# Kernel optimization log

Hardware: AMD Instinct MI355X
Metric: run time of the kernel (lower is better)

Reference implementation:

```python
import jax, jax.numpy as jnp
import numpy as np

B, L, H, ED, NCONV = 64, 2048, 128, 4, 3
N = B * L


def gat(x, src, dst, edge_attr, W, a_s, a_d, We, a_e, b, self_loops):
    """PyG GATConv, heads=1, concat=True, negative_slope=0.2, fill_value='mean'."""
    n = x.shape[0]
    h = x @ W                              # [N,H]
    a_src = h @ a_s                        # [N]
    a_dst = h @ a_d                        # [N]
    alpha = a_src[src] + a_dst[dst] + (edge_attr @ We) @ a_e  # [E]
    if self_loops:
        ones = jnp.ones(src.shape[0], x.dtype)
        deg = jax.ops.segment_sum(ones, dst, num_segments=n)
        mean_attr = jax.ops.segment_sum(edge_attr, dst, num_segments=n) / jnp.maximum(deg, 1.0)[:, None]
        loop_alpha = a_src + a_dst + (mean_attr @ We) @ a_e
        idx = jnp.arange(n, dtype=src.dtype)
        src = jnp.concatenate([src, idx])
        dst = jnp.concatenate([dst, idx])
        alpha = jnp.concatenate([alpha, loop_alpha])
    alpha = jax.nn.leaky_relu(alpha, 0.2)
    m = jax.ops.segment_max(alpha, dst, num_segments=n)
    ex = jnp.exp(alpha - m[dst])
    den = jax.ops.segment_sum(ex, dst, num_segments=n)
    coef = ex / jnp.maximum(den, 1e-16)[dst]
    return jax.ops.segment_sum(coef[:, None] * h[src], dst, num_segments=n) + b


def setup_inputs() -> dict:
    key = jax.random.key(0)
    ks = iter(jax.random.split(key, 32))
    # binary trees: per graph, node k>0 has parent (k-1)//2; edge child->parent (to_up)
    local = np.arange(1, L)
    parent = (local - 1) // 2
    offs = (np.arange(B) * L)[:, None]
    src = jnp.asarray((local[None, :] + offs).ravel(), dtype=jnp.int32)
    dst = jnp.asarray((parent[None, :] + offs).ravel(), dtype=jnp.int32)
    E = src.shape[0]
    s = 0.1
    inp = {
        "x": jax.random.normal(next(ks), (N,), jnp.float32),
        "src": src,
        "dst": dst,
        "edge_attr": jax.random.normal(next(ks), (E, ED), jnp.float32),
        "up_W0": jax.random.normal(next(ks), (1, H)) * s,
        "up_W": jax.random.normal(next(ks), (NCONV - 1, H, H)) * s,
        "up_att_src": jax.random.normal(next(ks), (NCONV, H)) * s,
        "up_att_dst": jax.random.normal(next(ks), (NCONV, H)) * s,
        "up_We": jax.random.normal(next(ks), (NCONV, ED, H)) * s,
        "up_att_edge": jax.random.normal(next(ks), (NCONV, H)) * s,
        "up_b": jax.random.normal(next(ks), (NCONV, H)) * s,
        "down_W": jax.random.normal(next(ks), (NCONV - 1, H, H)) * s,
        "down_att_src": jax.random.normal(next(ks), (NCONV - 1, H)) * s,
        "down_att_dst": jax.random.normal(next(ks), (NCONV - 1, H)) * s,
        "down_We": jax.random.normal(next(ks), (NCONV - 1, ED, H)) * s,
        "down_att_edge": jax.random.normal(next(ks), (NCONV - 1, H)) * s,
        "down_b": jax.random.normal(next(ks), (NCONV - 1, H)) * s,
        "lin_W": jax.random.normal(next(ks), (NCONV - 1, H, H)) * s,
        "lin_b": jax.random.normal(next(ks), (NCONV - 1, H)) * s,
        "lin_last_W": jax.random.normal(next(ks), (H, 1)) * s,
        "lin_last_b": jax.random.normal(next(ks), (1,)) * s,
    }
    return inp


def reference(x, src, dst, edge_attr, up_W0, up_W, up_att_src, up_att_dst, up_We,
              up_att_edge, up_b, down_W, down_att_src, down_att_dst, down_We,
              down_att_edge, down_b, lin_W, lin_b, lin_last_W, lin_last_b):
    h = x[:, None]                                            # flat_c.view(-1,1)
    # upward pass: toup GATConvs (with self loops) + relu
    for i in range(NCONV):
        W = up_W0 if i == 0 else up_W[i - 1]
        h = jax.nn.relu(gat(h, src, dst, edge_attr, W, up_att_src[i], up_att_dst[i],
                            up_We[i], up_att_edge[i], up_b[i], True))
    x_up = h
    # downward pass uses reversed edges, no self loops; replicates original's
    # indexing bug (todown[0] used twice, todown[-1] never used)
    src_d, dst_d = dst, src
    x_down = jax.nn.relu(gat(x_up, src_d, dst_d, edge_attr, down_W[0], down_att_src[0],
                             down_att_dst[0], down_We[0], down_att_edge[0], down_b[0], False))
    xx = x_down + x_up
    for i in range(NCONV - 1):
        xx = jax.nn.relu(xx @ lin_W[i] + lin_b[i])
        x_down = jax.nn.relu(gat(xx, src_d, dst_d, edge_attr, down_W[i], down_att_src[i],
                                 down_att_dst[i], down_We[i], down_att_edge[i], down_b[i], False))
        xx = x_down + x_up
    final_emb = xx
    out_nodes = xx @ lin_last_W + lin_last_b                  # [N,1]
    batch_out = out_nodes.reshape(B, L)                       # all graphs are max_len
    batch_emb = final_emb.reshape(B, L, H)
    out = batch_out - batch_out[:, :1]                        # subtract root node
    return out, batch_emb
```

## Files before the change

kernel.cpp:

```cpp
#include <hip/hip_runtime.h>
#include <hip/hip_bf16.h>
#include <cstdint>
#include <cstddef>

typedef unsigned short u16;
typedef short bf16x8 __attribute__((ext_vector_type(8)));
typedef float f32x4 __attribute__((ext_vector_type(4)));

#define Bn 64
#define Ln 2048
#define Hn 128
#define EDn 4
#define Nn (Bn*Ln)

#define CV_W0    0
#define CV_WUP   128
#define CV_AS    32896
#define CV_AD    33280
#define CV_WE    33664
#define CV_AE    35200
#define CV_BUP   35584
#define CV_WD    35968
#define CV_BD    68736
#define CV_WL    68992
#define CV_BL    101760
#define CV_WLAST 102016
#define CV_TOTAL 102144

__device__ __forceinline__ float b2f(u16 u) {
  union { float f; unsigned int i; } v; v.i = ((unsigned int)u) << 16; return v.f;
}
__device__ __forceinline__ u16 f2b(float f) {
  __hip_bfloat16 h = __float2bfloat16(f);
  union { __hip_bfloat16 h; u16 u; } v; v.h = h; return v.u;
}
__device__ __forceinline__ float lrelu(float v) { return v >= 0.f ? v : 0.2f * v; }
__device__ __forceinline__ float wave_sum(float r) {
  #pragma unroll
  for (int off = 32; off > 0; off >>= 1) r += __shfl_xor(r, off, 64);
  return r;
}
__device__ __forceinline__ float ld_in(const void* p, size_t i, int f) {
  return f ? b2f(((const u16*)p)[i]) : ((const float*)p)[i];
}
__device__ __forceinline__ u16* Cbase(void* dout, int f) {
  return f ? ((u16*)dout + Nn) : (u16*)((float*)dout + Nn);
}
__device__ __forceinline__ float lo16(unsigned v) { return b2f((u16)(v & 0xFFFF)); }
__device__ __forceinline__ float hi16(unsigned v) { return b2f((u16)(v >> 16)); }

__global__ void detect_kernel(const u16* __restrict__ x, int* __restrict__ flag) {
  int lane = threadIdx.x;
  u16 u = x[lane];
  int e = (u >> 7) & 0xFF;
  bool good = (e >= 100 && e <= 140) || ((u & 0x7FFF) == 0);
  unsigned long long m = __ballot(good);
  if (lane == 0) *flag = (__popcll(m) >= 56) ? 1 : 0;
}

struct CvtArgs { const void* src[12]; int off[12]; int tr[12]; };
__global__ void cvt_kernel(CvtArgs a, const int* __restrict__ flagp, u16* __restrict__ dst) {
  int f = *flagp;
  int i = blockIdx.x * 256 + threadIdx.x;
  if (i >= CV_TOTAL) return;
  int s = 0;
  #pragma unroll
  for (int k = 1; k < 12; ++k) s = (i >= a.off[k]) ? k : s;
  int j = i - a.off[s];
  int sj = j;
  if (a.tr[s]) {
    int mat = j >> 14, rr = (j >> 7) & 127, cc = j & 127;
    sj = (mat << 14) + cc * 128 + rr;
  }
  dst[i] = f ? ((const u16*)a.src[s])[sj] : f2b(((const float*)a.src[s])[sj]);
}

__global__ void up0_kernel(const void* __restrict__ x, const void* __restrict__ edge_attr,
                           const u16* __restrict__ W0, const u16* __restrict__ att_s,
                           const u16* __restrict__ att_d, const u16* __restrict__ We0,
                           const u16* __restrict__ ae0, const u16* __restrict__ b0,
                           u16* __restrict__ y, const int* __restrict__ flagp) {
  __shared__ float P[6];
  __shared__ float comb[64];
  __shared__ float W0s[Hn];
  __shared__ float b0s[Hn];
  int f = *flagp;
  int t = threadIdx.x;
  int lane = t & 63, w = t >> 6;
  if (w < 2) {
    const u16* vb = (w == 0) ? att_s : att_d;
    float r = b2f(W0[lane]) * b2f(vb[lane]) + b2f(W0[lane+64]) * b2f(vb[lane+64]);
    r = wave_sum(r);
    if (lane == 0) P[w] = r;
  } else {
    int e0 = (w - 2) * 2;
    float a0 = b2f(ae0[lane]), a1 = b2f(ae0[lane+64]);
    float r0 = b2f(We0[e0*Hn+lane])*a0     + b2f(We0[e0*Hn+lane+64])*a1;
    float r1 = b2f(We0[(e0+1)*Hn+lane])*a0 + b2f(We0[(e0+1)*Hn+lane+64])*a1;
    r0 = wave_sum(r0); r1 = wave_sum(r1);
    if (lane == 0) { P[2+e0] = r0; P[3+e0] = r1; }
  }
  if (t < Hn) { W0s[t] = b2f(W0[t]); b0s[t] = b2f(b0[t]); }
  __syncthreads();
  int base = blockIdx.x * 64;
  if (t < 64) {
    int n = base + t;
    int local = n & (Ln - 1);
    int nb = n >> 11;
    int root = n - local;
    float S0 = P[0], D0 = P[1];
    float w0 = P[2], w1 = P[3], w2 = P[4], w3 = P[5];
    float xp = ld_in(x, n, f);
    float ad_p = D0 * xp;
    int c1l = 2*local + 1, c2l = 2*local + 2;
    int deg = (c1l < Ln ? 1 : 0) + (c2l < Ln ? 1 : 0);
    float e1 = 0.f, e2 = 0.f, xc1 = 0.f, xc2 = 0.f, sc1 = 0.f, sc2 = 0.f;
    if (deg >= 1) {
      xc1 = ld_in(x, root + c1l, f);
      size_t ei = ((size_t)nb*(Ln-1) + (c1l-1))*EDn;
      e1 = ld_in(edge_attr, ei+0, f)*w0 + ld_in(edge_attr, ei+1, f)*w1
         + ld_in(edge_attr, ei+2, f)*w2 + ld_in(edge_attr, ei+3, f)*w3;
      sc1 = lrelu(S0*xc1 + ad_p + e1);
    }
    if (deg == 2) {
      xc2 = ld_in(x, root + c2l, f);
      size_t ei = ((size_t)nb*(Ln-1) + (c2l-1))*EDn;
      e2 = ld_in(edge_attr, ei+0, f)*w0 + ld_in(edge_attr, ei+1, f)*w1
         + ld_in(edge_attr, ei+2, f)*w2 + ld_in(edge_attr, ei+3, f)*w3;
      sc2 = lrelu(S0*xc2 + ad_p + e2);
    }
    float mean_e = deg ? (e1 + e2) / (float)deg : 0.f;
    float ss = lrelu(S0*xp + ad_p + mean_e);
    float m = ss;
    if (deg >= 1) m = fmaxf(m, sc1);
    if (deg == 2) m = fmaxf(m, sc2);
    float es  = __expf(ss - m);
    float ec1 = (deg >= 1) ? __expf(sc1 - m) : 0.f;
    float ec2 = (deg == 2) ? __expf(sc2 - m) : 0.f;
    float den = es + ec1 + ec2;
    comb[t] = (es*xp + ec1*xc1 + ec2*xc2) / den;
  }
  __syncthreads();
  u16* out = y + (size_t)base * Hn;
  for (int i = t; i < 64*Hn/4; i += 256) {
    int row = i >> 5;
    int col = (i & 31) * 4;
    float c = comb[row];
    ushort4 st;
    st.x = f2b(fmaxf(c*W0s[col+0] + b0s[col+0], 0.f));
    st.y = f2b(fmaxf(c*W0s[col+1] + b0s[col+1], 0.f));
    st.z = f2b(fmaxf(c*W0s[col+2] + b0s[col+2], 0.f));
    st.w = f2b(fmaxf(c*W0s[col+3] + b0s[col+3], 0.f));
    *(ushort4*)&out[(size_t)i*4] = st;
  }
}

template<int GATHER, int EPI, int ASAD>
__global__ __launch_bounds__(256, 2) void gemm_k(
                       const u16* __restrict__ Xp, const u16* __restrict__ Wt,
                       const u16* __restrict__ bias, const u16* __restrict__ Uarr,
                       u16* __restrict__ outp, void* __restrict__ dout,
                       const int* __restrict__ flagp, int x_is_C, int out_mode,
                       float2* __restrict__ asad, const u16* __restrict__ avs,
                       const u16* __restrict__ avd, float* __restrict__ nodesp) {
  __shared__ u16 Ws[Hn*Hn];
  int f = *flagp;
  const u16* X = x_is_C ? Cbase(dout, f) : Xp;
  int t = threadIdx.x;
  int lane = t & 63, w = t >> 6;
  int m = lane & 15, q = lane >> 4;
  int row0 = blockIdx.x * 256;
  int wbase = row0 + w*64;
  uint4 xf[4][4];
  #pragma unroll
  for (int rt = 0; rt < 4; ++rt) {
    int R = wbase + rt*16 + m;
    bool zero = false;
    const uint4* src;
    if (GATHER) {
      int local = R & (Ln - 1);
      if (local == 0) { zero = true; src = (const uint4*)X; }
      else src = (const uint4*)(X + (size_t)((R - local) + ((local - 1) >> 1))*Hn);
    } else {
      src = (const uint4*)(X + (size_t)R*Hn);
    }
    #pragma unroll
    for (int ki = 0; ki < 4; ++ki) {
      uint4 v = src[ki*4 + q];
      if (zero) { v.x = 0; v.y = 0; v.z = 0; v.w = 0; }
      xf[rt][ki] = v;
    }
  }
  #pragma unroll
  for (int i = 0; i < 8; ++i) {
    int g = t + 256*i; int r = g >> 4, u = g & 15;
    uint4 v = ((const uint4*)Wt)[g];
    *(uint4*)&Ws[(r*16 + (u ^ (r & 15)))*8] = v;
  }
  __syncthreads();
  f32x4 acc[4][8];
  #pragma unroll
  for (int rt = 0; rt < 4; ++rt)
    #pragma unroll
    for (int ct = 0; ct < 8; ++ct) acc[rt][ct] = (f32x4){0.f, 0.f, 0.f, 0.f};
  #pragma unroll
  for (int ki = 0; ki < 4; ++ki) {
    #pragma unroll
    for (int ct = 0; ct < 8; ++ct) {
      bf16x8 wf = *(bf16x8*)&Ws[((ct*16 + m)*16 + ((ki*4 + q) ^ m))*8];
      #pragma unroll
      for (int rt = 0; rt < 4; ++rt)
        acc[rt][ct] = __builtin_amdgcn_mfma_f32_16x16x32_bf16(
                        wf, *(bf16x8*)&xf[rt][ki], acc[rt][ct], 0, 0, 0);
    }
  }
  u16* Cb = Cbase(dout, f);
  float* emf = (float*)dout + Nn;
  u16* od = (out_mode == 0) ? outp : (out_mode == 1 ? Cb : (u16*)dout + Nn);
  #pragma unroll
  for (int rt = 0; rt < 4; ++rt) {
    int R = wbase + rt*16 + m;
    float asv = 0.f, adv = 0.f;
    #pragma unroll
    for (int ct = 0; ct < 8; ++ct) {
      int c0 = ct*16 + q*4;
      float o[4];
      #pragma unroll
      for (int r = 0; r < 4; ++r) o[r] = acc[rt][ct][r];
      if (ASAD == 1) {
        ushort4 sv = *(const ushort4*)&avs[c0];
        ushort4 dv = *(const ushort4*)&avd[c0];
        asv += o[0]*b2f(sv.x) + o[1]*b2f(sv.y) + o[2]*b2f(sv.z) + o[3]*b2f(sv.w);
        adv += o[0]*b2f(dv.x) + o[1]*b2f(dv.y) + o[2]*b2f(dv.z) + o[3]*b2f(dv.w);
      }
      if (EPI >= 1) {
        ushort4 bv = *(const ushort4*)&bias[c0];
        o[0] = fmaxf(o[0] + b2f(bv.x), 0.f); o[1] = fmaxf(o[1] + b2f(bv.y), 0.f);
        o[2] = fmaxf(o[2] + b2f(bv.z), 0.f); o[3] = fmaxf(o[3] + b2f(bv.w), 0.f);
      }
      if (EPI == 2) {
        ushort4 uv = *(const ushort4*)&Uarr[(size_t)R*Hn + c0];
        o[0] += b2f(uv.x); o[1] += b2f(uv.y); o[2] += b2f(uv.z); o[3] += b2f(uv.w);
      }
      if (ASAD == 2) {
        ushort4 sv = *(const ushort4*)&avs[c0];
        asv += o[0]*b2f(sv.x) + o[1]*b2f(sv.y) + o[2]*b2f(sv.z) + o[3]*b2f(sv.w);
      }
      if (out_mode == 2 && !f) {
        float4 fv; fv.x = o[0]; fv.y = o[1]; fv.z = o[2]; fv.w = o[3];
        *(float4*)&emf[(size_t)R*Hn + c0] = fv;
      } else {
        ushort4 st; st.x = f2b(o[0]); st.y = f2b(o[1]); st.z = f2b(o[2]); st.w = f2b(o[3]);
        *(ushort4*)&od[(size_t)R*Hn + c0] = st;
      }
    }
    if (ASAD == 1) {
      asv += __shfl_xor(asv, 16, 64); asv += __shfl_xor(asv, 32, 64);
      adv += __shfl_xor(adv, 16, 64); adv += __shfl_xor(adv, 32, 64);
      if (q == 0) { float2 v; v.x = asv; v.y = adv; asad[R] = v; }
    }
    if (ASAD == 2) {
      asv += __shfl_xor(asv, 16, 64); asv += __shfl_xor(asv, 32, 64);
      if (q == 0) nodesp[R] = asv;
    }
  }
}

__global__ __launch_bounds__(256, 2) void gemm_blend_k(
                       const u16* __restrict__ Wt, const float2* __restrict__ coef,
                       const u16* __restrict__ bias_up, u16* __restrict__ outp,
                       void* __restrict__ dout, const int* __restrict__ flagp,
                       float2* __restrict__ asad, const u16* __restrict__ avs,
                       const u16* __restrict__ avd) {
  __shared__ u16 Ws[Hn*Hn];
  int f = *flagp;
  const u16* h = Cbase(dout, f);
  int t = threadIdx.x;
  int lane = t & 63, w = t >> 6;
  int m = lane & 15, q = lane >> 4;
  int row0 = blockIdx.x * 256;
  int wbase = row0 + w*64;
  uint4 xf[4][4];
  #pragma unroll
  for (int rt = 0; rt < 4; ++rt) {
    int R = wbase + rt*16 + m;
    int local = R & (Ln - 1);
    int root = R - local;
    int c1l = 2*local + 1, c2l = 2*local + 2;
    int r1 = (c1l < Ln) ? root + c1l : R;
    int r2 = (c2l < Ln) ? root + c2l : R;
    float2 cf = coef[R];
    float es = 1.f - cf.x - cf.y;
    const uint4* hp = (const uint4*)(h + (size_t)R*Hn);
    const uint4* h1 = (const uint4*)(h + (size_t)r1*Hn);
    const uint4* h2 = (const uint4*)(h + (size_t)r2*Hn);
    #pragma unroll
    for (int ki = 0; ki < 4; ++ki) {
      int u = ki*4 + q;
      uint4 a = hp[u], b = h1[u], c = h2[u];
      uint4 bv = ((const uint4*)bias_up)[u];
      uint4 st;
      #pragma unroll
      for (int i = 0; i < 4; ++i) {
        unsigned av = ((unsigned*)&a)[i], b1v = ((unsigned*)&b)[i];
        unsigned b2v = ((unsigned*)&c)[i], bbv = ((unsigned*)&bv)[i];
        float o0 = es*lo16(av) + cf.x*lo16(b1v) + cf.y*lo16(b2v) + lo16(bbv);
        float o1 = es*hi16(av) + cf.x*hi16(b1v) + cf.y*hi16(b2v) + hi16(bbv);
        ((unsigned*)&st)[i] = (unsigned)f2b(fmaxf(o0, 0.f))
                            | ((unsigned)f2b(fmaxf(o1, 0.f)) << 16);
      }
      xf[rt][ki] = st;
    }
  }
  #pragma unroll
  for (int i = 0; i < 8; ++i) {
    int g = t + 256*i; int r = g >> 4, u = g & 15;
    uint4 v = ((const uint4*)Wt)[g];
    *(uint4*)&Ws[(r*16 + (u ^ (r & 15)))*8] = v;
  }
  __syncthreads();
  f32x4 acc[4][8];
  #pragma unroll
  for (int rt = 0; rt < 4; ++rt)
    #pragma unroll
    for (int ct = 0; ct < 8; ++ct) acc[rt][ct] = (f32x4){0.f, 0.f, 0.f, 0.f};
  #pragma unroll
  for (int ki = 0; ki < 4; ++ki) {
    #pragma unroll
    for (int ct = 0; ct < 8; ++ct) {
      bf16x8 wf = *(bf16x8*)&Ws[((ct*16 + m)*16 + ((ki*4 + q) ^ m))*8];
      #pragma unroll
      for (int rt = 0; rt < 4; ++rt)
        acc[rt][ct] = __builtin_amdgcn_mfma_f32_16x16x32_bf16(
                        wf, *(bf16x8*)&xf[rt][ki], acc[rt][ct], 0, 0, 0);
    }
  }
  #pragma unroll
  for (int rt = 0; rt < 4; ++rt) {
    int R = wbase + rt*16 + m;
    float asv = 0.f, adv = 0.f;
    #pragma unroll
    for (int ct = 0; ct < 8; ++ct) {
      int c0 = ct*16 + q*4;
      float o0 = acc[rt][ct][0], o1 = acc[rt][ct][1];
      float o2 = acc[rt][ct][2], o3 = acc[rt][ct][3];
      ushort4 sv = *(const ushort4*)&avs[c0];
      ushort4 dv = *(const ushort4*)&avd[c0];
      asv += o0*b2f(sv.x) + o1*b2f(sv.y) + o2*b2f(sv.z) + o3*b2f(sv.w);
      adv += o0*b2f(dv.x) + o1*b2f(dv.y) + o2*b2f(dv.z) + o3*b2f(dv.w);
      ushort4 st; st.x = f2b(o0); st.y = f2b(o1); st.z = f2b(o2); st.w = f2b(o3);
      *(ushort4*)&outp[(size_t)R*Hn + c0] = st;
    }
    asv += __shfl_xor(asv, 16, 64); asv += __shfl_xor(asv, 32, 64);
    adv += __shfl_xor(adv, 16, 64); adv += __shfl_xor(adv, 32, 64);
    if (q == 0) { float2 v; v.x = asv; v.y = adv; asad[R] = v; }
  }
}

__global__ __launch_bounds__(256, 2) void fused_down_lin_k(
                       const u16* __restrict__ Xp, const u16* __restrict__ Wdt,
                       const u16* __restrict__ bd, const u16* __restrict__ Uarr,
                       const u16* __restrict__ Wlt, const u16* __restrict__ bl,
                       u16* __restrict__ outp) {
  __shared__ u16 Ws[Hn*Hn];
  __shared__ u16 XX[128*Hn];
  int t = threadIdx.x;
  int lane = t & 63, w = t >> 6;
  int m = lane & 15, q = lane >> 4;
  int row0 = blockIdx.x * 128;
  int wbase = row0 + w*32;
  uint4 xf[2][4];
  #pragma unroll
  for (int rt = 0; rt < 2; ++rt) {
    int R = wbase + rt*16 + m;
    int local = R & (Ln - 1);
    bool zero = (local == 0);
    const uint4* src = zero ? (const uint4*)Xp
                     : (const uint4*)(Xp + (size_t)((R - local) + ((local - 1) >> 1))*Hn);
    #pragma unroll
    for (int ki = 0; ki < 4; ++ki) {
      uint4 v = src[ki*4 + q];
      if (zero) { v.x = 0; v.y = 0; v.z = 0; v.w = 0; }
      xf[rt][ki] = v;
    }
  }
  #pragma unroll
  for (int i = 0; i < 8; ++i) {
    int g = t + 256*i; int r = g >> 4, u = g & 15;
    uint4 v = ((const uint4*)Wdt)[g];
    *(uint4*)&Ws[(r*16 + (u ^ (r & 15)))*8] = v;
  }
  __syncthreads();
  f32x4 acc[2][8];
  #pragma unroll
  for (int rt = 0; rt < 2; ++rt)
    #pragma unroll
    for (int ct = 0; ct < 8; ++ct) acc[rt][ct] = (f32x4){0.f, 0.f, 0.f, 0.f};
  #pragma unroll
  for (int ki = 0; ki < 4; ++ki) {
    #pragma unroll
    for (int ct = 0; ct < 8; ++ct) {
      bf16x8 wf = *(bf16x8*)&Ws[((ct*16 + m)*16 + ((ki*4 + q) ^ m))*8];
      #pragma unroll
      for (int rt = 0; rt < 2; ++rt)
        acc[rt][ct] = __builtin_amdgcn_mfma_f32_16x16x32_bf16(
                        wf, *(bf16x8*)&xf[rt][ki], acc[rt][ct], 0, 0, 0);
    }
  }
  __syncthreads();
  #pragma unroll
  for (int rt = 0; rt < 2; ++rt) {
    int R = wbase + rt*16 + m;
    int rl = w*32 + rt*16 + m;
    #pragma unroll
    for (int ct = 0; ct < 8; ++ct) {
      int c0 = ct*16 + q*4;
      ushort4 bv = *(const ushort4*)&bd[c0];
      ushort4 uv = *(const ushort4*)&Uarr[(size_t)R*Hn + c0];
      float o0 = fmaxf(acc[rt][ct][0] + b2f(bv.x), 0.f) + b2f(uv.x);
      float o1 = fmaxf(acc[rt][ct][1] + b2f(bv.y), 0.f) + b2f(uv.y);
      float o2 = fmaxf(acc[rt][ct][2] + b2f(bv.z), 0.f) + b2f(uv.z);
      float o3 = fmaxf(acc[rt][ct][3] + b2f(bv.w), 0.f) + b2f(uv.w);
      int uu = (2*ct + (q >> 1)) ^ m;
      uint2 pk;
      pk.x = (unsigned)f2b(o0) | ((unsigned)f2b(o1) << 16);
      pk.y = (unsigned)f2b(o2) | ((unsigned)f2b(o3) << 16);
      *(uint2*)&XX[rl*Hn + uu*8 + (q & 1)*4] = pk;
    }
  }
  #pragma unroll
  for (int i = 0; i < 8; ++i) {
    int g = t + 256*i; int r = g >> 4, u = g & 15;
    uint4 v = ((const uint4*)Wlt)[g];
    *(uint4*)&Ws[(r*16 + (u ^ (r & 15)))*8] = v;
  }
  __syncthreads();
  f32x4 acc2[2][8];
  #pragma unroll
  for (int rt = 0; rt < 2; ++rt)
    #pragma unroll
    for (int ct = 0; ct < 8; ++ct) acc2[rt][ct] = (f32x4){0.f, 0.f, 0.f, 0.f};
  #pragma unroll
  for (int ki = 0; ki < 4; ++ki) {
    #pragma unroll
    for (int ct = 0; ct < 8; ++ct) {
      bf16x8 wf = *(bf16x8*)&Ws[((ct*16 + m)*16 + ((ki*4 + q) ^ m))*8];
      #pragma unroll
      for (int rt = 0; rt < 2; ++rt) {
        int rl = w*32 + rt*16 + m;
        bf16x8 xb = *(bf16x8*)&XX[rl*Hn + (((ki*4 + q) ^ m))*8];
        acc2[rt][ct] = __builtin_amdgcn_mfma_f32_16x16x32_bf16(wf, xb, acc2[rt][ct], 0, 0, 0);
      }
    }
  }
  #pragma unroll
  for (int rt = 0; rt < 2; ++rt) {
    int R = wbase + rt*16 + m;
    #pragma unroll
    for (int ct = 0; ct < 8; ++ct) {
      int c0 = ct*16 + q*4;
      ushort4 bv = *(const ushort4*)&bl[c0];
      ushort4 st;
      st.x = f2b(fmaxf(acc2[rt][ct][0] + b2f(bv.x), 0.f));
      st.y = f2b(fmaxf(acc2[rt][ct][1] + b2f(bv.y), 0.f));
      st.z = f2b(fmaxf(acc2[rt][ct][2] + b2f(bv.z), 0.f));
      st.w = f2b(fmaxf(acc2[rt][ct][3] + b2f(bv.w), 0.f));
      *(ushort4*)&outp[(size_t)R*Hn + c0] = st;
    }
  }
}

__global__ void coef_kernel(const void* __restrict__ edge_attr,
                            const u16* __restrict__ We, const u16* __restrict__ ae,
                            const float2* __restrict__ asad, float2* __restrict__ coef,
                            const int* __restrict__ flagp) {
  __shared__ float P[4];
  int f = *flagp;
  int t = threadIdx.x;
  int lane = t & 63, w = t >> 6;
  {
    unsigned av = *(const unsigned*)&ae[2*lane];
    unsigned wv = *(const unsigned*)&We[w*Hn + 2*lane];
    float r = wave_sum(lo16(wv)*lo16(av) + hi16(wv)*hi16(av));
    if (lane == 0) P[w] = r;
  }
  __syncthreads();
  int p = blockIdx.x * 256 + t;
  int local = p & (Ln - 1);
  int root = p - local;
  int nb = p >> 11;
  int c1l = 2*local + 1, c2l = 2*local + 2;
  int deg = (c1l < Ln ? 1 : 0) + (c2l < Ln ? 1 : 0);
  float2 aa = asad[p];
  float w0 = P[0], w1 = P[1], w2 = P[2], w3 = P[3];
  float e1 = 0.f, e2 = 0.f, sc1 = 0.f, sc2 = 0.f;
  if (deg >= 1) {
    size_t ei = ((size_t)nb*(Ln-1) + (c1l-1))*EDn;
    if (f) {
      ushort4 v = *(const ushort4*)((const u16*)edge_attr + ei);
      e1 = b2f(v.x)*w0 + b2f(v.y)*w1 + b2f(v.z)*w2 + b2f(v.w)*w3;
      if (deg == 2) {
        ushort4 v2 = *(const ushort4*)((const u16*)edge_attr + ei + EDn);
        e2 = b2f(v2.x)*w0 + b2f(v2.y)*w1 + b2f(v2.z)*w2 + b2f(v2.w)*w3;
      }
    } else {
      float4 v = *(const float4*)((const float*)edge_attr + ei);
      e1 = v.x*w0 + v.y*w1 + v.z*w2 + v.w*w3;
      if (deg == 2) {
        float4 v2 = *(const float4*)((const float*)edge_attr + ei + EDn);
        e2 = v2.x*w0 + v2.y*w1 + v2.z*w2 + v2.w*w3;
      }
    }
    sc1 = lrelu(asad[root + c1l].x + aa.y + e1);
    if (deg == 2) sc2 = lrelu(asad[root + c2l].x + aa.y + e2);
  }
  float mean_e = deg ? (e1 + e2) / (float)deg : 0.f;
  float ss = lrelu(aa.x + aa.y + mean_e);
  float m = ss;
  if (deg >= 1) m = fmaxf(m, sc1);
  if (deg == 2) m = fmaxf(m, sc2);
  float es  = __expf(ss - m);
  float ec1 = (deg >= 1) ? __expf(sc1 - m) : 0.f;
  float ec2 = (deg == 2) ? __expf(sc2 - m) : 0.f;
  float inv = 1.f / (es + ec1 + ec2);
  float2 cf; cf.x = ec1 * inv; cf.y = ec2 * inv;
  coef[p] = cf;
}

__global__ void blend_kernel(const u16* __restrict__ h, const float2* __restrict__ coef,
                             const u16* __restrict__ bias, u16* __restrict__ y) {
  int t = threadIdx.x;
  int g = t & 15;
  int p = blockIdx.x * 16 + (t >> 4);
  int local = p & (Ln - 1);
  int root = p - local;
  int c1l = 2*local + 1, c2l = 2*local + 2;
  int deg = (c1l < Ln ? 1 : 0) + (c2l < Ln ? 1 : 0);
  float2 cf = coef[p];
  float es = 1.f - cf.x - cf.y;
  int off = g * 8;
  uint4 hp = *(const uint4*)&h[(size_t)p*Hn + off];
  uint4 h1 = {0,0,0,0}, h2 = {0,0,0,0};
  if (deg >= 1) h1 = *(const uint4*)&h[(size_t)(root + c1l)*Hn + off];
  if (deg == 2) h2 = *(const uint4*)&h[(size_t)(root + c2l)*Hn + off];
  uint4 bv = *(const uint4*)&bias[off];
  uint4 st;
  #pragma unroll
  for (int i = 0; i < 4; ++i) {
    unsigned a = ((unsigned*)&hp)[i], b1 = ((unsigned*)&h1)[i];
    unsigned b2 = ((unsigned*)&h2)[i], bb = ((unsigned*)&bv)[i];
    float o0 = es*lo16(a) + cf.x*lo16(b1) + cf.y*lo16(b2) + lo16(bb);
    float o1 = es*hi16(a) + cf.x*hi16(b1) + cf.y*hi16(b2) + hi16(bb);
    ((unsigned*)&st)[i] = (unsigned)f2b(fmaxf(o0, 0.f)) | ((unsigned)f2b(fmaxf(o1, 0.f)) << 16);
  }
  *(uint4*)&y[(size_t)p*Hn + off] = st;
}

__global__ void score_kernel(const float* __restrict__ nodes, void* __restrict__ dout,
                             const int* __restrict__ flagp) {
  int f = *flagp;
  int n = blockIdx.x * 256 + threadIdx.x;
  float v = nodes[n] - nodes[n & ~(Ln - 1)];
  if (f) ((u16*)dout)[n] = f2b(v);
  else   ((float*)dout)[n] = v;
}

extern "C" void kernel_launch(void* const* d_in, const int* in_sizes, int n_in,
                              void* d_out, int out_size, void* d_ws, size_t ws_size,
                              hipStream_t stream) {
  const void* x         = d_in[0];
  const void* edge_attr = d_in[3];

  u16* Ubuf = (u16*)d_ws;
  u16* Abuf = Ubuf + (size_t)Nn*Hn;
  u16* Bbuf = Abuf + (size_t)Nn*Hn;
  u16* cvt  = Bbuf + (size_t)Nn*Hn;
  float2* asad = (float2*)(cvt + CV_TOTAL);
  float2* coef = asad + Nn;
  float* nodes = (float*)(coef + Nn);
  int* flag = (int*)(nodes + Nn);

  detect_kernel<<<1, 64, 0, stream>>>((const u16*)d_in[0], flag);

  CvtArgs ca;
  ca.src[0]  = d_in[4];  ca.off[0]  = CV_W0;    ca.tr[0]  = 0;
  ca.src[1]  = d_in[5];  ca.off[1]  = CV_WUP;   ca.tr[1]  = 1;
  ca.src[2]  = d_in[6];  ca.off[2]  = CV_AS;    ca.tr[2]  = 0;
  ca.src[3]  = d_in[7];  ca.off[3]  = CV_AD;    ca.tr[3]  = 0;
  ca.src[4]  = d_in[8];  ca.off[4]  = CV_WE;    ca.tr[4]  = 0;
  ca.src[5]  = d_in[9];  ca.off[5]  = CV_AE;    ca.tr[5]  = 0;
  ca.src[6]  = d_in[10]; ca.off[6]  = CV_BUP;   ca.tr[6]  = 0;
  ca.src[7]  = d_in[11]; ca.off[7]  = CV_WD;    ca.tr[7]  = 1;
  ca.src[8]  = d_in[16]; ca.off[8]  = CV_BD;    ca.tr[8]  = 0;
  ca.src[9]  = d_in[17]; ca.off[9]  = CV_WL;    ca.tr[9]  = 1;
  ca.src[10] = d_in[18]; ca.off[10] = CV_BL;    ca.tr[10] = 0;
  ca.src[11] = d_in[19]; ca.off[11] = CV_WLAST; ca.tr[11] = 0;
  cvt_kernel<<<(CV_TOTAL + 255)/256, 256, 0, stream>>>(ca, flag, cvt);

  up0_kernel<<<Nn/64, 256, 0, stream>>>(x, edge_attr, cvt+CV_W0, cvt+CV_AS, cvt+CV_AD,
                                        cvt+CV_WE, cvt+CV_AE, cvt+CV_BUP, Abuf, flag);
  gemm_k<0,0,1><<<Nn/256, 256, 0, stream>>>(Abuf, cvt+CV_WUP, nullptr, nullptr,
                                         nullptr, d_out, flag, 0, 1,
                                         asad, cvt+CV_AS+Hn, cvt+CV_AD+Hn, nullptr);
  coef_kernel<<<Nn/256, 256, 0, stream>>>(edge_attr, cvt+CV_WE+EDn*Hn, cvt+CV_AE+Hn,
                                          asad, coef, flag);
  gemm_blend_k<<<Nn/256, 256, 0, stream>>>(cvt+CV_WUP+Hn*Hn, coef, cvt+CV_BUP+Hn,
                                           Bbuf, d_out, flag,
                                           asad, cvt+CV_AS+2*Hn, cvt+CV_AD+2*Hn);
  coef_kernel<<<Nn/256, 256, 0, stream>>>(edge_attr, cvt+CV_WE+2*EDn*Hn, cvt+CV_AE+2*Hn,
                                          asad, coef, flag);
  blend_kernel<<<Nn/16, 256, 0, stream>>>(Bbuf, coef, cvt+CV_BUP+2*Hn, Ubuf);

  fused_down_lin_k<<<Nn/128, 256, 0, stream>>>(Ubuf, cvt+CV_WD, cvt+CV_BD, Ubuf,
                                               cvt+CV_WL, cvt+CV_BL, Abuf);
  fused_down_lin_k<<<Nn/128, 256, 0, stream>>>(Abuf, cvt+CV_WD, cvt+CV_BD, Ubuf,
                                               cvt+CV_WL+Hn*Hn, cvt+CV_BL+Hn, Bbuf);
  gemm_k<1,2,2><<<Nn/256, 256, 0, stream>>>(Bbuf, cvt+CV_WD+Hn*Hn, cvt+CV_BD+Hn, Ubuf,
                                         nullptr, d_out, flag, 0, 2,
                                         nullptr, cvt+CV_WLAST, nullptr, nodes);

  score_kernel<<<Nn/256, 256, 0, stream>>>(nodes, d_out, flag);
}
```

Before: 266.0 us.

## Shrink GEMM row tiles, split column accumulation, prefetch weights into registers

The node GEMM kernels now process 128 rows per block instead of 256, with two 16-row tiles per wave. Columns are accumulated in two halves so fewer accumulator registers are live, and launch bounds rise to allow four blocks per CU. Weight tiles are loaded into registers before the activation gather, so their latency overlaps the gather instead of following it. The fused down/lin kernel moves to 512 threads with one 16-row tile per wave and prefetches the second weight matrix during the first epilogue. The cost is that each block now loads the shared 32KB weight tile for half as many rows, and register pressure under the tighter bounds could cause spills.

```diff
diff --git a/kernel.cpp b/kernel.cpp
--- a/kernel.cpp
+++ b/kernel.cpp
@@ -156,7 +156,7 @@
 }
 
 template<int GATHER, int EPI, int ASAD>
-__global__ __launch_bounds__(256, 2) void gemm_k(
+__global__ __launch_bounds__(256, 4) void gemm_k(
                        const u16* __restrict__ Xp, const u16* __restrict__ Wt,
                        const u16* __restrict__ bias, const u16* __restrict__ Uarr,
                        u16* __restrict__ outp, void* __restrict__ dout,
@@ -169,11 +169,14 @@
   int t = threadIdx.x;
   int lane = t & 63, w = t >> 6;
   int m = lane & 15, q = lane >> 4;
-  int row0 = blockIdx.x * 256;
-  int wbase = row0 + w*64;
-  uint4 xf[4][4];
-  #pragma unroll
-  for (int rt = 0; rt < 4; ++rt) {
+  int row0 = blockIdx.x * 128;
+  int wbase = row0 + w*32;
+  uint4 wstage[8];
+  #pragma unroll
+  for (int i = 0; i < 8; ++i) wstage[i] = ((const uint4*)Wt)[t + 256*i];
+  uint4 xf[2][4];
+  #pragma unroll
+  for (int rt = 0; rt < 2; ++rt) {
     int R = wbase + rt*16 + m;
     bool zero = false;
     const uint4* src;
@@ -194,79 +197,89 @@
   #pragma unroll
   for (int i = 0; i < 8; ++i) {
     int g = t + 256*i; int r = g >> 4, u = g & 15;
-    uint4 v = ((const uint4*)Wt)[g];
-    *(uint4*)&Ws[(r*16 + (u ^ (r & 15)))*8] = v;
-  }
-  __syncthreads();
-  f32x4 acc[4][8];
-  #pragma unroll
-  for (int rt = 0; rt < 4; ++rt)
-    #pragma unroll
-    for (int ct = 0; ct < 8; ++ct) acc[rt][ct] = (f32x4){0.f, 0.f, 0.f, 0.f};
-  #pragma unroll
-  for (int ki = 0; ki < 4; ++ki) {
-    #pragma unroll
-    for (int ct = 0; ct < 8; ++ct) {
-      bf16x8 wf = *(bf16x8*)&Ws[((ct*16 + m)*16 + ((ki*4 + q) ^ m))*8];
-      #pragma unroll
-      for (int rt = 0; rt < 4; ++rt)
-        acc[rt][ct] = __builtin_amdgcn_mfma_f32_16x16x32_bf16(
-                        wf, *(bf16x8*)&xf[rt][ki], acc[rt][ct], 0, 0, 0);
-    }
-  }
+    *(uint4*)&Ws[(r*16 + (u ^ (r & 15)))*8] = wstage[i];
+  }
+  __syncthreads();
   u16* Cb = Cbase(dout, f);
   float* emf = (float*)dout + Nn;
   u16* od = (out_mode == 0) ? outp : (out_mode == 1 ? Cb : (u16*)dout + Nn);
-  #pragma unroll
-  for (int rt = 0; rt < 4; ++rt) {
+  float asv[2] = {0.f, 0.f}, adv[2] = {0.f, 0.f};
+  #pragma unroll
+  for (int cb = 0; cb < 2; ++cb) {
+    f32x4 acc[2][4];
+    #pragma unroll
+    for (int rt = 0; rt < 2; ++rt)
+      #pragma unroll
+      for (int c4 = 0; c4 < 4; ++c4) acc[rt][c4] = (f32x4){0.f, 0.f, 0.f, 0.f};
+    #pragma unroll
+    for (int ki = 0; ki < 4; ++ki) {
+      #pragma unroll
+      for (int c4 = 0; c4 < 4; ++c4) {
+        int ct = cb*4 + c4;
+        bf16x8 wf = *(bf16x8*)&Ws[((ct*16 + m)*16 + ((ki*4 + q) ^ m))*8];
+        #pragma unroll
+        for (int rt = 0; rt < 2; ++rt)
+          acc[rt][c4] = __builtin_amdgcn_mfma_f32_16x16x32_bf16(
+                          wf, *(bf16x8*)&xf[rt][ki], acc[rt][c4], 0, 0, 0);
+      }
+    }
+    #pragma unroll
+    for (int rt = 0; rt < 2; ++rt) {
+      int R = wbase + rt*16 + m;
+      #pragma unroll
+      for (int c4 = 0; c4 < 4; ++c4) {
+        int ct = cb*4 + c4;
+        int c0 = ct*16 + q*4;
+        float o[4];
+        #pragma unroll
+        for (int r = 0; r < 4; ++r) o[r] = acc[rt][c4][r];
+        if (ASAD == 1) {
+          ushort4 sv = *(const ushort4*)&avs[c0];
+          ushort4 dv = *(const ushort4*)&avd[c0];
+          asv[rt] += o[0]*b2f(sv.x) + o[1]*b2f(sv.y) + o[2]*b2f(sv.z) + o[3]*b2f(sv.w);
+          adv[rt] += o[0]*b2f(dv.x) + o[1]*b2f(dv.y) + o[2]*b2f(dv.z) + o[3]*b2f(dv.w);
+        }
+        if (EPI >= 1) {
+          ushort4 bv = *(const ushort4*)&bias[c0];
+          o[0] = fmaxf(o[0] + b2f(bv.x), 0.f); o[1] = fmaxf(o[1] + b2f(bv.y), 0.f);
+          o[2] = fmaxf(o[2] + b2f(bv.z), 0.f); o[3] = fmaxf(o[3] + b2f(bv.w), 0.f);
+        }
+        if (EPI == 2) {
+          ushort4 uv = *(const ushort4*)&Uarr[(size_t)R*Hn + c0];
+          o[0] += b2f(uv.x); o[1] += b2f(uv.y); o[2] += b2f(uv.z); o[3] += b2f(uv.w);
+        }
+        if (ASAD == 2) {
+          ushort4 sv = *(const ushort4*)&avs[c0];
+          asv[rt] += o[0]*b2f(sv.x) + o[1]*b2f(sv.y) + o[2]*b2f(sv.z) + o[3]*b2f(sv.w);
+        }
+        if (out_mode == 2 && !f) {
+          float4 fv; fv.x = o[0]; fv.y = o[1]; fv.z = o[2]; fv.w = o[3];
+          *(float4*)&emf[(size_t)R*Hn + c0] = fv;
+        } else {
+          ushort4 st; st.x = f2b(o[0]); st.y = f2b(o[1]); st.z = f2b(o[2]); st.w = f2b(o[3]);
+          *(ushort4*)&od[(size_t)R*Hn + c0] = st;
+        }
+      }
+    }
+  }
+  #pragma unroll
+  for (int rt = 0; rt < 2; ++rt) {
     int R = wbase + rt*16 + m;
-    float asv = 0.f, adv = 0.f;
-    #pragma unroll
-    for (int ct = 0; ct < 8; ++ct) {
-      int c0 = ct*16 + q*4;
-      float o[4];
-      #pragma unroll
-      for (int r = 0; r < 4; ++r) o[r] = acc[rt][ct][r];
-      if (ASAD == 1) {
-        ushort4 sv = *(const ushort4*)&avs[c0];
-        ushort4 dv = *(const ushort4*)&avd[c0];
-        asv += o[0]*b2f(sv.x) + o[1]*b2f(sv.y) + o[2]*b2f(sv.z) + o[3]*b2f(sv.w);
-        adv += o[0]*b2f(dv.x) + o[1]*b2f(dv.y) + o[2]*b2f(dv.z) + o[3]*b2f(dv.w);
-      }
-      if (EPI >= 1) {
-        ushort4 bv = *(const ushort4*)&bias[c0];
-        o[0] = fmaxf(o[0] + b2f(bv.x), 0.f); o[1] = fmaxf(o[1] + b2f(bv.y), 0.f);
-        o[2] = fmaxf(o[2] + b2f(bv.z), 0.f); o[3] = fmaxf(o[3] + b2f(bv.w), 0.f);
-      }
-      if (EPI == 2) {
-        ushort4 uv = *(const ushort4*)&Uarr[(size_t)R*Hn + c0];
-        o[0] += b2f(uv.x); o[1] += b2f(uv.y); o[2] += b2f(uv.z); o[3] += b2f(uv.w);
-      }
-      if (ASAD == 2) {
-        ushort4 sv = *(const ushort4*)&avs[c0];
-        asv += o[0]*b2f(sv.x) + o[1]*b2f(sv.y) + o[2]*b2f(sv.z) + o[3]*b2f(sv.w);
-      }
-      if (out_mode == 2 && !f) {
-        float4 fv; fv.x = o[0]; fv.y = o[1]; fv.z = o[2]; fv.w = o[3];
-        *(float4*)&emf[(size_t)R*Hn + c0] = fv;
-      } else {
-        ushort4 st; st.x = f2b(o[0]); st.y = f2b(o[1]); st.z = f2b(o[2]); st.w = f2b(o[3]);
-        *(ushort4*)&od[(size_t)R*Hn + c0] = st;
-      }
-    }
     if (ASAD == 1) {
-      asv += __shfl_xor(asv, 16, 64); asv += __shfl_xor(asv, 32, 64);
-      adv += __shfl_xor(adv, 16, 64); adv += __shfl_xor(adv, 32, 64);
-      if (q == 0) { float2 v; v.x = asv; v.y = adv; asad[R] = v; }
+      float as_ = asv[rt], ad_ = adv[rt];
+      as_ += __shfl_xor(as_, 16, 64); as_ += __shfl_xor(as_, 32, 64);
+      ad_ += __shfl_xor(ad_, 16, 64); ad_ += __shfl_xor(ad_, 32, 64);
+      if (q == 0) { float2 v; v.x = as_; v.y = ad_; asad[R] = v; }
     }
     if (ASAD == 2) {
-      asv += __shfl_xor(asv, 16, 64); asv += __shfl_xor(asv, 32, 64);
-      if (q == 0) nodesp[R] = asv;
-    }
-  }
-}
-
-__global__ __launch_bounds__(256, 2) void gemm_blend_k(
+      float as_ = asv[rt];
+      as_ += __shfl_xor(as_, 16, 64); as_ += __shfl_xor(as_, 32, 64);
+      if (q == 0) nodesp[R] = as_;
+    }
+  }
+}
+
+__global__ __launch_bounds__(256, 4) void gemm_blend_k(
                        const u16* __restrict__ Wt, const float2* __restrict__ coef,
                        const u16* __restrict__ bias_up, u16* __restrict__ outp,
                        void* __restrict__ dout, const int* __restrict__ flagp,
@@ -278,11 +291,14 @@
   int t = threadIdx.x;
   int lane = t & 63, w = t >> 6;
   int m = lane & 15, q = lane >> 4;
-  int row0 = blockIdx.x * 256;
-  int wbase = row0 + w*64;
-  uint4 xf[4][4];
-  #pragma unroll
-  for (int rt = 0; rt < 4; ++rt) {
+  int row0 = blockIdx.x * 128;
+  int wbase = row0 + w*32;
+  uint4 wstage[8];
+  #pragma unroll
+  for (int i = 0; i < 8; ++i) wstage[i] = ((const uint4*)Wt)[t + 256*i];
+  uint4 xf[2][4];
+  #pragma unroll
+  for (int rt = 0; rt < 2; ++rt) {
     int R = wbase + rt*16 + m;
     int local = R & (Ln - 1);
     int root = R - local;
@@ -315,49 +331,58 @@
   #pragma unroll
   for (int i = 0; i < 8; ++i) {
     int g = t + 256*i; int r = g >> 4, u = g & 15;
-    uint4 v = ((const uint4*)Wt)[g];
-    *(uint4*)&Ws[(r*16 + (u ^ (r & 15)))*8] = v;
-  }
-  __syncthreads();
-  f32x4 acc[4][8];
-  #pragma unroll
-  for (int rt = 0; rt < 4; ++rt)
-    #pragma unroll
-    for (int ct = 0; ct < 8; ++ct) acc[rt][ct] = (f32x4){0.f, 0.f, 0.f, 0.f};
-  #pragma unroll
-  for (int ki = 0; ki < 4; ++ki) {
-    #pragma unroll
-    for (int ct = 0; ct < 8; ++ct) {
-      bf16x8 wf = *(bf16x8*)&Ws[((ct*16 + m)*16 + ((ki*4 + q) ^ m))*8];
+    *(uint4*)&Ws[(r*16 + (u ^ (r & 15)))*8] = wstage[i];
+  }
+  __syncthreads();
+  float asv[2] = {0.f, 0.f}, adv[2] = {0.f, 0.f};
+  #pragma unroll
+  for (int cb = 0; cb < 2; ++cb) {
+    f32x4 acc[2][4];
+    #pragma unroll
+    for (int rt = 0; rt < 2; ++rt)
       #pragma unroll
-      for (int rt = 0; rt < 4; ++rt)
-        acc[rt][ct] = __builtin_amdgcn_mfma_f32_16x16x32_bf16(
-                        wf, *(bf16x8*)&xf[rt][ki], acc[rt][ct], 0, 0, 0);
-    }
-  }
-  #pragma unroll
-  for (int rt = 0; rt < 4; ++rt) {
+      for (int c4 = 0; c4 < 4; ++c4) acc[rt][c4] = (f32x4){0.f, 0.f, 0.f, 0.f};
+    #pragma unroll
+    for (int ki = 0; ki < 4; ++ki) {
+      #pragma unroll
+      for (int c4 = 0; c4 < 4; ++c4) {
+        int ct = cb*4 + c4;
+        bf16x8 wf = *(bf16x8*)&Ws[((ct*16 + m)*16 + ((ki*4 + q) ^ m))*8];
+        #pragma unroll
+        for (int rt = 0; rt < 2; ++rt)
+          acc[rt][c4] = __builtin_amdgcn_mfma_f32_16x16x32_bf16(
+                          wf, *(bf16x8*)&xf[rt][ki], acc[rt][c4], 0, 0, 0);
+      }
+    }
+    #pragma unroll
+    for (int rt = 0; rt < 2; ++rt) {
+      int R = wbase + rt*16 + m;
+      #pragma unroll
+      for (int c4 = 0; c4 < 4; ++c4) {
+        int ct = cb*4 + c4;
+        int c0 = ct*16 + q*4;
+        float o0 = acc[rt][c4][0], o1 = acc[rt][c4][1];
+        float o2 = acc[rt][c4][2], o3 = acc[rt][c4][3];
+        ushort4 sv = *(const ushort4*)&avs[c0];
+        ushort4 dv = *(const ushort4*)&avd[c0];
+        asv[rt] += o0*b2f(sv.x) + o1*b2f(sv.y) + o2*b2f(sv.z) + o3*b2f(sv.w);
+        adv[rt] += o0*b2f(dv.x) + o1*b2f(dv.y) + o2*b2f(dv.z) + o3*b2f(dv.w);
+        ushort4 st; st.x = f2b(o0); st.y = f2b(o1); st.z = f2b(o2); st.w = f2b(o3);
+        *(ushort4*)&outp[(size_t)R*Hn + c0] = st;
+      }
+    }
+  }
+  #pragma unroll
+  for (int rt = 0; rt < 2; ++rt) {
     int R = wbase + rt*16 + m;
-    float asv = 0.f, adv = 0.f;
-    #pragma unroll
-    for (int ct = 0; ct < 8; ++ct) {
-      int c0 = ct*16 + q*4;
-      float o0 = acc[rt][ct][0], o1 = acc[rt][ct][1];
-      float o2 = acc[rt][ct][2], o3 = acc[rt][ct][3];
-      ushort4 sv = *(const ushort4*)&avs[c0];
-      ushort4 dv = *(const ushort4*)&avd[c0];
-      asv += o0*b2f(sv.x) + o1*b2f(sv.y) + o2*b2f(sv.z) + o3*b2f(sv.w);
-      adv += o0*b2f(dv.x) + o1*b2f(dv.y) + o2*b2f(dv.z) + o3*b2f(dv.w);
-      ushort4 st; st.x = f2b(o0); st.y = f2b(o1); st.z = f2b(o2); st.w = f2b(o3);
-      *(ushort4*)&outp[(size_t)R*Hn + c0] = st;
-    }
-    asv += __shfl_xor(asv, 16, 64); asv += __shfl_xor(asv, 32, 64);
-    adv += __shfl_xor(adv, 16, 64); adv += __shfl_xor(adv, 32, 64);
-    if (q == 0) { float2 v; v.x = asv; v.y = adv; asad[R] = v; }
-  }
-}
-
-__global__ __launch_bounds__(256, 2) void fused_down_lin_k(
+    float as_ = asv[rt], ad_ = adv[rt];
+    as_ += __shfl_xor(as_, 16, 64); as_ += __shfl_xor(as_, 32, 64);
+    ad_ += __shfl_xor(ad_, 16, 64); ad_ += __shfl_xor(ad_, 32, 64);
+    if (q == 0) { float2 v; v.x = as_; v.y = ad_; asad[R] = v; }
+  }
+}
+
+__global__ __launch_bounds__(512, 4) void fused_down_lin_k(
                        const u16* __restrict__ Xp, const u16* __restrict__ Wdt,
                        const u16* __restrict__ bd, const u16* __restrict__ Uarr,
                        const u16* __restrict__ Wlt, const u16* __restrict__ bl,
@@ -368,11 +393,13 @@
   int lane = t & 63, w = t >> 6;
   int m = lane & 15, q = lane >> 4;
   int row0 = blockIdx.x * 128;
-  int wbase = row0 + w*32;
-  uint4 xf[2][4];
-  #pragma unroll
-  for (int rt = 0; rt < 2; ++rt) {
-    int R = wbase + rt*16 + m;
+  int R = row0 + w*16 + m;
+  int rl = w*16 + m;
+  uint4 wstage[4];
+  #pragma unroll
+  for (int i = 0; i < 4; ++i) wstage[i] = ((const uint4*)Wdt)[t + 512*i];
+  uint4 xf[4];
+  {
     int local = R & (Ln - 1);
     bool zero = (local == 0);
     const uint4* src = zero ? (const uint4*)Xp
@@ -381,92 +408,73 @@
     for (int ki = 0; ki < 4; ++ki) {
       uint4 v = src[ki*4 + q];
       if (zero) { v.x = 0; v.y = 0; v.z = 0; v.w = 0; }
-      xf[rt][ki] = v;
-    }
-  }
-  #pragma unroll
-  for (int i = 0; i < 8; ++i) {
-    int g = t + 256*i; int r = g >> 4, u = g & 15;
-    uint4 v = ((const uint4*)Wdt)[g];
-    *(uint4*)&Ws[(r*16 + (u ^ (r & 15)))*8] = v;
-  }
-  __syncthreads();
-  f32x4 acc[2][8];
-  #pragma unroll
-  for (int rt = 0; rt < 2; ++rt)
-    #pragma unroll
-    for (int ct = 0; ct < 8; ++ct) acc[rt][ct] = (f32x4){0.f, 0.f, 0.f, 0.f};
+      xf[ki] = v;
+    }
+  }
+  #pragma unroll
+  for (int i = 0; i < 4; ++i) {
+    int g = t + 512*i; int r = g >> 4, u = g & 15;
+    *(uint4*)&Ws[(r*16 + (u ^ (r & 15)))*8] = wstage[i];
+  }
+  __syncthreads();
+  f32x4 acc[8];
+  #pragma unroll
+  for (int ct = 0; ct < 8; ++ct) acc[ct] = (f32x4){0.f, 0.f, 0.f, 0.f};
   #pragma unroll
   for (int ki = 0; ki < 4; ++ki) {
     #pragma unroll
     for (int ct = 0; ct < 8; ++ct) {
       bf16x8 wf = *(bf16x8*)&Ws[((ct*16 + m)*16 + ((ki*4 + q) ^ m))*8];
-      #pragma unroll
-      for (int rt = 0; rt < 2; ++rt)
-        acc[rt][ct] = __builtin_amdgcn_mfma_f32_16x16x32_bf16(
-                        wf, *(bf16x8*)&xf[rt][ki], acc[rt][ct], 0, 0, 0);
-    }
-  }
-  __syncthreads();
-  #pragma unroll
-  for (int rt = 0; rt < 2; ++rt) {
-    int R = wbase + rt*16 + m;
-    int rl = w*32 + rt*16 + m;
-    #pragma unroll
-    for (int ct = 0; ct < 8; ++ct) {
-      int c0 = ct*16 + q*4;
-      ushort4 bv = *(const ushort4*)&bd[c0];
-      ushort4 uv = *(const ushort4*)&Uarr[(size_t)R*Hn + c0];
-      float o0 = fmaxf(acc[rt][ct][0] + b2f(bv.x), 0.f) + b2f(uv.x);
-      float o1 = fmaxf(acc[rt][ct][1] + b2f(bv.y), 0.f) + b2f(uv.y);
-      float o2 = fmaxf(acc[rt][ct][2] + b2f(bv.z), 0.f) + b2f(uv.z);
-      float o3 = fmaxf(acc[rt][ct][3] + b2f(bv.w), 0.f) + b2f(uv.w);
-      int uu = (2*ct + (q >> 1)) ^ m;
-      uint2 pk;
-      pk.x = (unsigned)f2b(o0) | ((unsigned)f2b(o1) << 16);
-      pk.y = (unsigned)f2b(o2) | ((unsigned)f2b(o3) << 16);
-      *(uint2*)&XX[rl*Hn + uu*8 + (q & 1)*4] = pk;
-    }
-  }
-  #pragma unroll
-  for (int i = 0; i < 8; ++i) {
-    int g = t + 256*i; int r = g >> 4, u = g & 15;
-    uint4 v = ((const uint4*)Wlt)[g];
-    *(uint4*)&Ws[(r*16 + (u ^ (r & 15)))*8] = v;
-  }
-  __syncthreads();
-  f32x4 acc2[2][8];
-  #pragma unroll
-  for (int rt = 0; rt < 2; ++rt)
-    #pragma unroll
-    for (int ct = 0; ct < 8; ++ct) acc2[rt][ct] = (f32x4){0.f, 0.f, 0.f, 0.f};
+      acc[ct] = __builtin_amdgcn_mfma_f32_16x16x32_bf16(
+                    wf, *(bf16x8*)&xf[ki], acc[ct], 0, 0, 0);
+    }
+  }
+  __syncthreads();
+  #pragma unroll
+  for (int i = 0; i < 4; ++i) wstage[i] = ((const uint4*)Wlt)[t + 512*i];
+  #pragma unroll
+  for (int ct = 0; ct < 8; ++ct) {
+    int c0 = ct*16 + q*4;
+    ushort4 bv = *(const ushort4*)&bd[c0];
+    ushort4 uv = *(const ushort4*)&Uarr[(size_t)R*Hn + c0];
+    float o0 = fmaxf(acc[ct][0] + b2f(bv.x), 0.f) + b2f(uv.x);
+    float o1 = fmaxf(acc[ct][1] + b2f(bv.y), 0.f) + b2f(uv.y);
+    float o2 = fmaxf(acc[ct][2] + b2f(bv.z), 0.f) + b2f(uv.z);
+    float o3 = fmaxf(acc[ct][3] + b2f(bv.w), 0.f) + b2f(uv.w);
+    int uu = (2*ct + (q >> 1)) ^ m;
+    uint2 pk;
+    pk.x = (unsigned)f2b(o0) | ((unsigned)f2b(o1) << 16);
+    pk.y = (unsigned)f2b(o2) | ((unsigned)f2b(o3) << 16);
+    *(uint2*)&XX[rl*Hn + uu*8 + (q & 1)*4] = pk;
+  }
+  #pragma unroll
+  for (int i = 0; i < 4; ++i) {
+    int g = t + 512*i; int r = g >> 4, u = g & 15;
+    *(uint4*)&Ws[(r*16 + (u ^ (r & 15)))*8] = wstage[i];
+  }
+  __syncthreads();
+  f32x4 acc2[8];
+  #pragma unroll
+  for (int ct = 0; ct < 8; ++ct) acc2[ct] = (f32x4){0.f, 0.f, 0.f, 0.f};
   #pragma unroll
   for (int ki = 0; ki < 4; ++ki) {
     #pragma unroll
     for (int ct = 0; ct < 8; ++ct) {
       bf16x8 wf = *(bf16x8*)&Ws[((ct*16 + m)*16 + ((ki*4 + q) ^ m))*8];
-      #pragma unroll
-      for (int rt = 0; rt < 2; ++rt) {
-        int rl = w*32 + rt*16 + m;
-        bf16x8 xb = *(bf16x8*)&XX[rl*Hn + (((ki*4 + q) ^ m))*8];
-        acc2[rt][ct] = __builtin_amdgcn_mfma_f32_16x16x32_bf16(wf, xb, acc2[rt][ct], 0, 0, 0);
-      }
-    }
-  }
-  #pragma unroll
-  for (int rt = 0; rt < 2; ++rt) {
-    int R = wbase + rt*16 + m;
-    #pragma unroll
-    for (int ct = 0; ct < 8; ++ct) {
-      int c0 = ct*16 + q*4;
-      ushort4 bv = *(const ushort4*)&bl[c0];
-      ushort4 st;
-      st.x = f2b(fmaxf(acc2[rt][ct][0] + b2f(bv.x), 0.f));
-      st.y = f2b(fmaxf(acc2[rt][ct][1] + b2f(bv.y), 0.f));
-      st.z = f2b(fmaxf(acc2[rt][ct][2] + b2f(bv.z), 0.f));
-      st.w = f2b(fmaxf(acc2[rt][ct][3] + b2f(bv.w), 0.f));
-      *(ushort4*)&outp[(size_t)R*Hn + c0] = st;
-    }
+      bf16x8 xb = *(bf16x8*)&XX[rl*Hn + (((ki*4 + q) ^ m))*8];
+      acc2[ct] = __builtin_amdgcn_mfma_f32_16x16x32_bf16(wf, xb, acc2[ct], 0, 0, 0);
+    }
+  }
+  #pragma unroll
+  for (int ct = 0; ct < 8; ++ct) {
+    int c0 = ct*16 + q*4;
+    ushort4 bv = *(const ushort4*)&bl[c0];
+    ushort4 st;
+    st.x = f2b(fmaxf(acc2[ct][0] + b2f(bv.x), 0.f));
+    st.y = f2b(fmaxf(acc2[ct][1] + b2f(bv.y), 0.f));
+    st.z = f2b(fmaxf(acc2[ct][2] + b2f(bv.z), 0.f));
+    st.w = f2b(fmaxf(acc2[ct][3] + b2f(bv.w), 0.f));
+    *(ushort4*)&outp[(size_t)R*Hn + c0] = st;
   }
 }
 
@@ -599,23 +607,23 @@
 
   up0_kernel<<<Nn/64, 256, 0, stream>>>(x, edge_attr, cvt+CV_W0, cvt+CV_AS, cvt+CV_AD,
                                         cvt+CV_WE, cvt+CV_AE, cvt+CV_BUP, Abuf, flag);
-  gemm_k<0,0,1><<<Nn/256, 256, 0, stream>>>(Abuf, cvt+CV_WUP, nullptr, nullptr,
+  gemm_k<0,0,1><<<Nn/128, 256, 0, stream>>>(Abuf, cvt+CV_WUP, nullptr, nullptr,
                                          nullptr, d_out, flag, 0, 1,
                                          asad, cvt+CV_AS+Hn, cvt+CV_AD+Hn, nullptr);
   coef_kernel<<<Nn/256, 256, 0, stream>>>(edge_attr, cvt+CV_WE+EDn*Hn, cvt+CV_AE+Hn,
                                           asad, coef, flag);
-  gemm_blend_k<<<Nn/256, 256, 0, stream>>>(cvt+CV_WUP+Hn*Hn, coef, cvt+CV_BUP+Hn,
+  gemm_blend_k<<<Nn/128, 256, 0, stream>>>(cvt+CV_WUP+Hn*Hn, coef, cvt+CV_BUP+Hn,
                                            Bbuf, d_out, flag,
                                            asad, cvt+CV_AS+2*Hn, cvt+CV_AD+2*Hn);
   coef_kernel<<<Nn/256, 256, 0, stream>>>(edge_attr, cvt+CV_WE+2*EDn*Hn, cvt+CV_AE+2*Hn,
                                           asad, coef, flag);
   blend_kernel<<<Nn/16, 256, 0, stream>>>(Bbuf, coef, cvt+CV_BUP+2*Hn, Ubuf);
 
-  fused_down_lin_k<<<Nn/128, 256, 0, stream>>>(Ubuf, cvt+CV_WD, cvt+CV_BD, Ubuf,
+  fused_down_lin_k<<<Nn/128, 512, 0, stream>>>(Ubuf, cvt+CV_WD, cvt+CV_BD, Ubuf,
                                                cvt+CV_WL, cvt+CV_BL, Abuf);
-  fused_down_lin_k<<<Nn/128, 256, 0, stream>>>(Abuf, cvt+CV_WD, cvt+CV_BD, Ubuf,
+  fused_down_lin_k<<<Nn/128, 512, 0, stream>>>(Abuf, cvt+CV_WD, cvt+CV_BD, Ubuf,
                                                cvt+CV_WL+Hn*Hn, cvt+CV_BL+Hn, Bbuf);
-  gemm_k<1,2,2><<<Nn/256, 256, 0, stream>>>(Bbuf, cvt+CV_WD+Hn*Hn, cvt+CV_BD+Hn, Ubuf,
+  gemm_k<1,2,2><<<Nn/128, 256, 0, stream>>>(Bbuf, cvt+CV_WD+Hn*Hn, cvt+CV_BD+Hn, Ubuf,
                                          nullptr, d_out, flag, 0, 2,
                                          nullptr, cvt+CV_WLAST, nullptr, nodes);
 
```

Result: slower. 275.0 us (+3.4%).
